# Optimization experiments

Hardware: AMD Instinct MI355X
Metric: run time of the kernel (lower is better)

Reference implementation:

```python
import jax, jax.numpy as jnp
import numpy as np

C = 27
SIZE = 448
PATCH = 14
G = PATCH * 4          # target_global = 56
SHN = (SIZE * SIZE) // (PATCH * PATCH)  # split_head_num = 1024
PW, GW = 0.75, 0.25    # patch_weight, global_weight
EPS = 1e-5


def setup_inputs() -> dict:
    key = jax.random.key(0)
    ks = jax.random.split(key, 9)
    s = 0.02
    return {
        "x": jax.random.normal(ks[0], (4, C, SIZE, SIZE), dtype=jnp.float32),
        "gn_w": jnp.ones((C,), jnp.float32),
        "gn_b": jnp.zeros((C,), jnp.float32),
        "q_w": jax.random.normal(ks[1], (C, C), jnp.float32) * s,
        "q_b": jax.random.normal(ks[2], (C,), jnp.float32) * s,
        "k_w": jax.random.normal(ks[3], (C, C), jnp.float32) * s,
        "k_b": jax.random.normal(ks[4], (C,), jnp.float32) * s,
        "v_w": jax.random.normal(ks[5], (C, C), jnp.float32) * s,
        "v_b": jax.random.normal(ks[6], (C,), jnp.float32) * s,
        "proj_w": jax.random.normal(ks[7], (C, C), jnp.float32) * s,
    }


def _conv1x1(w, bias, t):
    out = jnp.einsum('oc,bchw->bohw', w, t)
    return out if bias is None else out + bias[None, :, None, None]


def _bmm_attn(q, k, v, scale):
    # q,k,v: (b, d, n). w = softmax(q^T k * scale, axis=2); h = einsum over keys.
    w = jax.nn.softmax(jnp.einsum('bdn,bdm->bnm', q, k) * scale, axis=2)
    return jnp.einsum('bdj,bij->bdi', v, w)


def reference(x, gn_w, gn_b, q_w, q_b, k_w, k_b, v_w, v_b, proj_w):
    b, c, H, W = x.shape
    # GroupNorm(num_groups=1): normalize over (C,H,W) per sample
    mu = jnp.mean(x, axis=(1, 2, 3), keepdims=True)
    var = jnp.var(x, axis=(1, 2, 3), keepdims=True)
    xn = (x - mu) * jax.lax.rsqrt(var + EPS)
    xn = xn * gn_w[None, :, None, None] + gn_b[None, :, None, None]

    q = _conv1x1(q_w, q_b, xn)
    k = _conv1x1(k_w, k_b, xn)
    v = _conv1x1(v_w, v_b, xn)

    # AdaptiveAvgPool2d 448 -> 56 (exact factor 8): block mean
    f = H // G
    pool = lambda t: t.reshape(b, c, G, f, G, f).mean(axis=(3, 5))

    # patch-wise bmm attention: view (b, c*SHN, PATCH^2), attend over 196 positions
    d = c * SHN
    n = PATCH * PATCH
    qf = q.reshape(b, d, n)
    kf = k.reshape(b, d, n)
    vf = v.reshape(b, d, n)
    h_patch = _bmm_attn(qf, kf, vf, 1.0 / np.sqrt(d).astype(np.float32)).reshape(b, c, H, W)

    # global pooled bmm attention over 56*56 positions with dim c, then nearest upsample
    qg = pool(q).reshape(b, c, G * G)
    kg = pool(k).reshape(b, c, G * G)
    vg = pool(v).reshape(b, c, G * G)
    hg = _bmm_attn(qg, kg, vg, 1.0 / np.sqrt(c).astype(np.float32)).reshape(b, c, G, G)
    hg = jnp.repeat(jnp.repeat(hg, f, axis=2), f, axis=3)  # nearest upsample to (H, W)

    h_in = PW * h_patch + GW * hg
    return x + _conv1x1(proj_w, None, h_in)
```

## Files before the change

### kernel.cpp

```cpp
#include <hip/hip_runtime.h>
#include <hip/hip_bf16.h>
#include <cstdint>

namespace {
constexpr int BB = 4;
constexpr int CC = 27;
constexpr int HW = 448 * 448;
constexpr long long CHW = (long long)CC * HW;
constexpr int NP = 196;
constexpr int GG = 56 * 56;
constexpr int DTOT = CC * 1024;
constexpr float SCALE_P = 0.0060140449f;
constexpr float SCALE_G = 0.1924500897f;
constexpr float EPSV = 1e-5f;
constexpr int KCH = 512;
constexpr int NKS = DTOT / KCH;
constexpr int MPAD = 224;
constexpr int ROWB = 128;
constexpr int WFRAG = 7 * 13 * 64 * 8;
constexpr int XST = 40;
constexpr int GKC = 224;
constexpr int KST = 40;
constexpr int VST = 232;
constexpr int HST = 204;
}

typedef __attribute__((ext_vector_type(8))) short short8;
typedef __attribute__((ext_vector_type(4))) float f32x4;

__device__ __forceinline__ float bf2f(unsigned short u) {
    return __uint_as_float(((uint32_t)u) << 16);
}

__device__ __forceinline__ ushort f2bf(float f) {
    union { __hip_bfloat16 h; ushort u; } cv;
    cv.h = __float2bfloat16(f);
    return cv.u;
}

__global__ void k_fold(const float* __restrict__ pjw, const float* __restrict__ vw,
                       const float* __restrict__ vb, float* __restrict__ pvw,
                       float* __restrict__ pvb) {
    __shared__ float pj[729], vv[729], vbs[27];
    int t = threadIdx.x;
    for (int i = t; i < 729; i += 256) { pj[i] = pjw[i]; vv[i] = vw[i]; }
    if (t < 27) vbs[t] = vb[t];
    __syncthreads();
    for (int i = t; i < 729; i += 256) {
        int o = i / 27, c2 = i - (i / 27) * 27;
        float s = 0.f;
#pragma unroll
        for (int c = 0; c < 27; c++) s += pj[o * 27 + c] * vv[c * 27 + c2];
        pvw[i] = s;
    }
    if (t < 27) {
        float s = 0.f;
#pragma unroll
        for (int c = 0; c < 27; c++) s += pj[t * 27 + c] * vbs[c];
        pvb[t] = s;
    }
}

__global__ void k_gn_partial(const float* __restrict__ x, float* __restrict__ part) {
    int blk = blockIdx.x;
    int b = blk >> 10;
    int chunk = blk & 1023;
    const int CLEN = (int)(CHW / 1024);
    const float* p = x + (size_t)b * CHW + (size_t)chunk * CLEN;
    float s = 0.f, ss = 0.f;
    for (int i = threadIdx.x; i < CLEN; i += 256) {
        float v = p[i];
        s += v; ss += v * v;
    }
    for (int o = 32; o; o >>= 1) { s += __shfl_down(s, o); ss += __shfl_down(ss, o); }
    __shared__ float ls[4], lss[4];
    int wid = threadIdx.x >> 6, lane = threadIdx.x & 63;
    if (lane == 0) { ls[wid] = s; lss[wid] = ss; }
    __syncthreads();
    if (threadIdx.x == 0) {
        float S = ls[0] + ls[1] + ls[2] + ls[3];
        float SS = lss[0] + lss[1] + lss[2] + lss[3];
        part[blk * 2] = S; part[blk * 2 + 1] = SS;
    }
}

__global__ void k_gn_final(const float* __restrict__ part, float* __restrict__ stats) {
    int b = blockIdx.x;
    float s = 0.f, ss = 0.f;
    for (int i = threadIdx.x; i < 1024; i += 256) {
        s += part[(b * 1024 + i) * 2];
        ss += part[(b * 1024 + i) * 2 + 1];
    }
    for (int o = 32; o; o >>= 1) { s += __shfl_down(s, o); ss += __shfl_down(ss, o); }
    __shared__ float ls[4], lss[4];
    int wid = threadIdx.x >> 6, lane = threadIdx.x & 63;
    if (lane == 0) { ls[wid] = s; lss[wid] = ss; }
    __syncthreads();
    if (threadIdx.x == 0) {
        float S = ls[0] + ls[1] + ls[2] + ls[3];
        float SS = lss[0] + lss[1] + lss[2] + lss[3];
        float mean = S / (float)CHW;
        float var = SS / (float)CHW - mean * mean;
        stats[b * 2] = mean;
        stats[b * 2 + 1] = rsqrtf(var + EPSV);
    }
}

__global__ __launch_bounds__(256, 2)
void k_qkv_mfma(const float* __restrict__ x, const float* __restrict__ stats,
                const float* __restrict__ qw, const float* __restrict__ qb,
                const float* __restrict__ kw, const float* __restrict__ kb,
                const float* __restrict__ vw, const float* __restrict__ vb,
                const float* __restrict__ gnw, const float* __restrict__ gnb,
                __hip_bfloat16* __restrict__ qkv) {
    __shared__ ushort xs[256 * XST];
    __shared__ ushort wls[96 * XST];
    __shared__ __align__(16) float bls[96];
    __shared__ float gwls[27], gbls[27];

    int tid = threadIdx.x;
    int P0 = blockIdx.x * 256;
    int b = P0 / HW;
    int hw0 = P0 - b * HW;

    for (int i = tid; i < 96 * 32; i += 256) {
        int row = i >> 5, c = i & 31;
        float wv = 0.f;
        if (c < 27 && row < 81) {
            int t = (row >= 54) ? 2 : (row >= 27 ? 1 : 0);
            int oc = row - t * 27;
            const float* wp = (t == 0) ? qw : (t == 1) ? kw : vw;
            wv = wp[oc * 27 + c];
        }
        wls[row * XST + c] = f2bf(wv);
    }
    if (tid < 96) {
        float bv = 0.f;
        if (tid < 27) bv = qb[tid];
        else if (tid < 54) bv = kb[tid - 27];
        else if (tid < 81) bv = vb[tid - 54];
        bls[tid] = bv;
    }
    if (tid < 27) { gwls[tid] = gnw[tid]; gbls[tid] = gnb[tid]; }
    float mean = stats[b * 2], rstd = stats[b * 2 + 1];
    __syncthreads();

    {
        const float* xp = x + (size_t)b * CHW + hw0 + tid;
        ushort xv[28];
#pragma unroll
        for (int c = 0; c < 27; c++) {
            float v = (xp[(size_t)c * HW] - mean) * rstd * gwls[c] + gbls[c];
            xv[c] = f2bf(v);
        }
        xv[27] = 0;
        uint32_t* xrow = reinterpret_cast<uint32_t*>(&xs[tid * XST]);
#pragma unroll
        for (int i = 0; i < 14; i++)
            xrow[i] = (uint32_t)xv[2 * i] | ((uint32_t)xv[2 * i + 1] << 16);
        xrow[14] = 0; xrow[15] = 0;
    }
    __syncthreads();

    int w = tid >> 6, l = tid & 63;
    int lrow = l & 15, kg = l >> 4;

    short8 afr[6];
    f32x4 binit[6];
#pragma unroll
    for (int mt = 0; mt < 6; mt++) {
        afr[mt] = *reinterpret_cast<const short8*>(&wls[(mt * 16 + lrow) * XST + kg * 8]);
        binit[mt] = *reinterpret_cast<const f32x4*>(&bls[mt * 16 + kg * 4]);
    }

    f32x4 acc[4][6];
#pragma unroll
    for (int pt = 0; pt < 4; pt++) {
        const short8 bfr = *reinterpret_cast<const short8*>(
            &xs[(w * 64 + pt * 16 + lrow) * XST + kg * 8]);
#pragma unroll
        for (int mt = 0; mt < 6; mt++)
            acc[pt][mt] = __builtin_amdgcn_mfma_f32_16x16x32_bf16(afr[mt], bfr, binit[mt], 0, 0, 0);
    }

    ushort* ob = (ushort*)qkv;
#pragma unroll
    for (int pt = 0; pt < 4; pt++) {
        int hw = hw0 + w * 64 + pt * 16 + lrow;
#pragma unroll
        for (int mt = 0; mt < 6; mt++) {
#pragma unroll
            for (int r = 0; r < 4; r++) {
                int o = mt * 16 + kg * 4 + r;
                if (o < 81) {
                    int t = (o >= 54) ? 2 : (o >= 27 ? 1 : 0);
                    int oc = o - t * 27;
                    ob[((size_t)t * BB + b) * CHW + (size_t)oc * HW + hw] = f2bf(acc[pt][mt][r]);
                }
            }
        }
    }
}

__global__ void k_pool(const __hip_bfloat16* __restrict__ src, float* __restrict__ dst) {
    int idx = blockIdx.x * 256 + threadIdx.x;
    int g = idx % GG;
    int t = idx / GG;
    int c = t % 27;
    int b = t / 27;
    int gh = g / 56, gw = g - (g / 56) * 56;
    const ushort* sp = (const ushort*)src + (size_t)(b * 27 + c) * HW + (size_t)(gh * 8) * 448 + gw * 8;
    float s = 0.f;
#pragma unroll
    for (int r = 0; r < 8; r++) {
        const ushort4 a = *reinterpret_cast<const ushort4*>(sp + r * 448);
        const ushort4 d = *reinterpret_cast<const ushort4*>(sp + r * 448 + 4);
        s += bf2f(a.x) + bf2f(a.y) + bf2f(a.z) + bf2f(a.w)
           + bf2f(d.x) + bf2f(d.y) + bf2f(d.z) + bf2f(d.w);
    }
    dst[((size_t)b * GG + g) * 27 + c] = s * (1.f / 64.f);
}

__global__ __launch_bounds__(448, 1)
void k_spart_mfma(const __hip_bfloat16* __restrict__ q, const __hip_bfloat16* __restrict__ k,
                  float* __restrict__ spart) {
    __shared__ ushort lq[MPAD * 64];
    __shared__ ushort lk[MPAD * 64];
    int blk = blockIdx.x;
    int ks = blk % NKS;
    int b = blk / NKS;
    const ushort* qb_ = (const ushort*)q + (size_t)b * CHW;
    const ushort* kb_ = (const ushort*)k + (size_t)b * CHW;
    int t = threadIdx.x;
    int w = t >> 6, l = t & 63;
    int lrow = l & 15, lg = l >> 4;
    int sr = t & 15;
    int sn8 = t >> 4;

    f32x4 acc[2][13];
#pragma unroll
    for (int i = 0; i < 2; i++)
#pragma unroll
        for (int ct = 0; ct < 13; ct++) acc[i][ct] = (f32x4){0.f, 0.f, 0.f, 0.f};

    int d0 = ks * KCH;
    for (int step = 0; step < KCH / 32; ++step) {
        int dbase = d0 + step * 32;
        {
            const ushort* s0 = qb_ + (size_t)(dbase + 2 * sr) * NP + sn8 * 8;
            const ushort* s1 = s0 + NP;
            ushort4 a0 = *reinterpret_cast<const ushort4*>(s0);
            ushort4 a1 = *reinterpret_cast<const ushort4*>(s0 + 4);
            ushort4 b0 = *reinterpret_cast<const ushort4*>(s1);
            ushort4 b1 = *reinterpret_cast<const ushort4*>(s1 + 4);
            ushort ra[8] = {a0.x, a0.y, a0.z, a0.w, a1.x, a1.y, a1.z, a1.w};
            ushort rb[8] = {b0.x, b0.y, b0.z, b0.w, b1.x, b1.y, b1.z, b1.w};
#pragma unroll
            for (int kk = 0; kk < 8; kk++) {
                int n = sn8 * 8 + kk;
                uint32_t val = (uint32_t)ra[kk] | ((uint32_t)rb[kk] << 16);
                *reinterpret_cast<uint32_t*>(reinterpret_cast<char*>(lq) + n * ROWB +
                                             ((4 * sr) ^ (16 * (n & 7)))) = val;
            }
        }
        {
            const ushort* s0 = kb_ + (size_t)(dbase + 2 * sr) * NP + sn8 * 8;
            const ushort* s1 = s0 + NP;
            ushort4 a0 = *reinterpret_cast<const ushort4*>(s0);
            ushort4 a1 = *reinterpret_cast<const ushort4*>(s0 + 4);
            ushort4 b0 = *reinterpret_cast<const ushort4*>(s1);
            ushort4 b1 = *reinterpret_cast<const ushort4*>(s1 + 4);
            ushort ra[8] = {a0.x, a0.y, a0.z, a0.w, a1.x, a1.y, a1.z, a1.w};
            ushort rb[8] = {b0.x, b0.y, b0.z, b0.w, b1.x, b1.y, b1.z, b1.w};
#pragma unroll
            for (int kk = 0; kk < 8; kk++) {
                int m = sn8 * 8 + kk;
                uint32_t val = (uint32_t)ra[kk] | ((uint32_t)rb[kk] << 16);
                *reinterpret_cast<uint32_t*>(reinterpret_cast<char*>(lk) + m * ROWB +
                                             ((4 * sr) ^ (16 * (m & 7)))) = val;
            }
        }
        __syncthreads();
        int nA0 = (2 * w) * 16 + lrow;
        int nA1 = nA0 + 16;
        const short8 afr0 = *reinterpret_cast<const short8*>(
            reinterpret_cast<const char*>(lq) + nA0 * ROWB + 16 * (lg ^ (nA0 & 7)));
        const short8 afr1 = *reinterpret_cast<const short8*>(
            reinterpret_cast<const char*>(lq) + nA1 * ROWB + 16 * (lg ^ (nA1 & 7)));
#pragma unroll
        for (int ct = 0; ct < 13; ct++) {
            int m = ct * 16 + lrow;
            const short8 bfr = *reinterpret_cast<const short8*>(
                reinterpret_cast<const char*>(lk) + m * ROWB + 16 * (lg ^ (m & 7)));
            acc[0][ct] = __builtin_amdgcn_mfma_f32_16x16x32_bf16(afr0, bfr, acc[0][ct], 0, 0, 0);
            acc[1][ct] = __builtin_amdgcn_mfma_f32_16x16x32_bf16(afr1, bfr, acc[1][ct], 0, 0, 0);
        }
        __syncthreads();
    }
    float* sp = spart + (size_t)(b * NKS + ks) * NP * MPAD;
#pragma unroll
    for (int i = 0; i < 2; i++) {
        int rt = 2 * w + i;
#pragma unroll
        for (int r = 0; r < 4; r++) {
            int n = rt * 16 + lg * 4 + r;
            if (n < NP) {
#pragma unroll
                for (int ct = 0; ct < 13; ct++)
                    sp[(size_t)n * MPAD + ct * 16 + lrow] = acc[i][ct][r];
            }
        }
    }
}

__global__ void k_softmax(const float* __restrict__ spart, __hip_bfloat16* __restrict__ whf) {
    int blk = blockIdx.x;
    int n = blk % NP;
    int b = blk / NP;
    int m = threadIdx.x;
    float val = -1e30f;
    if (m < 196) {
        float s = 0.f;
        for (int ks = 0; ks < NKS; ks++)
            s += spart[((size_t)(b * NKS + ks) * NP + n) * MPAD + m];
        val = s * SCALE_P;
    }
    float mx = val;
    for (int o = 32; o; o >>= 1) mx = fmaxf(mx, __shfl_xor(mx, o));
    __shared__ float redm[4], reds[4];
    int wid = threadIdx.x >> 6, lane = threadIdx.x & 63;
    if (lane == 0) redm[wid] = mx;
    __syncthreads();
    mx = fmaxf(fmaxf(redm[0], redm[1]), fmaxf(redm[2], redm[3]));
    float p = (m < 196) ? __expf(val - mx) : 0.f;
    float sm = p;
    for (int o = 32; o; o >>= 1) sm += __shfl_xor(sm, o);
    if (lane == 0) reds[wid] = sm;
    __syncthreads();
    sm = reds[0] + reds[1] + reds[2] + reds[3];
    if (m < 224) {
        int ct = n >> 4, lr = n & 15;
        int step = m >> 5, kg = (m >> 3) & 3, e = m & 7;
        size_t addr = (size_t)b * WFRAG +
                      (((size_t)(step * 13 + ct) * 64 + kg * 16 + lr) << 3) + e;
        whf[addr] = __float2bfloat16((m < 196) ? p / sm : 0.f);
    }
}

__global__ __launch_bounds__(256)
void k_gattn_flash(const float* __restrict__ qg, const float* __restrict__ kg,
                   const float* __restrict__ vg, float* __restrict__ hg) {
    __shared__ __align__(16) ushort ksh[GKC * KST];
    __shared__ __align__(16) ushort vsh[32 * VST];
    __shared__ __align__(16) ushort psh[4][16 * VST];

    int blk = blockIdx.x;
    int b = blk / 49;
    int q0 = (blk % 49) * 64;
    int tid = threadIdx.x;
    int w = tid >> 6, l = tid & 63;
    int lr = l & 15, lg = l >> 4;

    for (int i = tid; i < GKC; i += 256) {
        ushort* kr = &ksh[i * KST];
        kr[27] = 0; kr[28] = 0; kr[29] = 0; kr[30] = 0; kr[31] = 0;
        vsh[27 * VST + i] = 0x3f80;
        vsh[28 * VST + i] = 0; vsh[29 * VST + i] = 0;
        vsh[30 * VST + i] = 0; vsh[31 * VST + i] = 0;
    }

    short8 aq;
    {
        const float* qr = qg + ((size_t)b * GG + q0 + w * 16 + lr) * 27;
#pragma unroll
        for (int j = 0; j < 8; j++) {
            int c = 8 * lg + j;
            aq[j] = (c < 27) ? (short)f2bf(qr[c]) : (short)0;
        }
    }

    f32x4 acc_h0 = {0.f, 0.f, 0.f, 0.f};
    f32x4 acc_h1 = {0.f, 0.f, 0.f, 0.f};
    ushort* myps = &psh[w][0];
    const float* kgb = kg + (size_t)b * GG * 27;
    const float* vgb = vg + (size_t)b * GG * 27;

    for (int ch = 0; ch < 14; ch++) {
        __syncthreads();
        int base = ch * GKC * 27;
        for (int idx = tid; idx < GKC * 27; idx += 256) {
            int kk = idx / 27, c = idx - (idx / 27) * 27;
            ksh[kk * KST + c] = f2bf(kgb[base + idx]);
            vsh[c * VST + kk] = f2bf(vgb[base + idx]);
        }
        __syncthreads();

        f32x4 s[14];
#pragma unroll
        for (int ct = 0; ct < 14; ct++) {
            const short8 bk = *reinterpret_cast<const short8*>(
                &ksh[(ct * 16 + lr) * KST + 8 * lg]);
            s[ct] = __builtin_amdgcn_mfma_f32_16x16x32_bf16(
                aq, bk, (f32x4){0.f, 0.f, 0.f, 0.f}, 0, 0, 0);
        }
#pragma unroll
        for (int ct = 0; ct < 14; ct++) {
#pragma unroll
            for (int r = 0; r < 4; r++) {
                float p = __expf(s[ct][r] * SCALE_G);
                myps[(4 * lg + r) * VST + ct * 16 + lr] = f2bf(p);
            }
        }
#pragma unroll
        for (int kstep = 0; kstep < 7; kstep++) {
            const short8 ap = *reinterpret_cast<const short8*>(
                &myps[lr * VST + kstep * 32 + 8 * lg]);
            const short8 bv0 = *reinterpret_cast<const short8*>(
                &vsh[lr * VST + kstep * 32 + 8 * lg]);
            const short8 bv1 = *reinterpret_cast<const short8*>(
                &vsh[(16 + lr) * VST + kstep * 32 + 8 * lg]);
            acc_h0 = __builtin_amdgcn_mfma_f32_16x16x32_bf16(ap, bv0, acc_h0, 0, 0, 0);
            acc_h1 = __builtin_amdgcn_mfma_f32_16x16x32_bf16(ap, bv1, acc_h1, 0, 0, 0);
        }
    }

#pragma unroll
    for (int r = 0; r < 4; r++) {
        float lsum = __shfl(acc_h1[r], (l & 48) | 11, 64);
        float inv = 1.f / lsum;
        int q = q0 + w * 16 + 4 * lg + r;
        float* hr = hg + ((size_t)b * GG + q) * 27;
        hr[lr] = acc_h0[r] * inv;
        if (lr < 11) hr[16 + lr] = acc_h1[r] * inv;
    }
}

__global__ __launch_bounds__(256)
void k_hp_fused(const __hip_bfloat16* __restrict__ v, const __hip_bfloat16* __restrict__ whf,
                const float* __restrict__ x, const float* __restrict__ hg,
                float* __restrict__ out) {
    __shared__ __align__(16) ushort hbuf[64 * HST];
    int blk = blockIdx.x;
    int b = blk / 432;
    int grp = blk % 432;
    int tid = threadIdx.x;
    int w = tid >> 6, l = tid & 63;
    int ar = l & 15;
    int kg = l >> 4;
    int D0 = (grp * 4 + w) * 16;

    const ushort* vb = (const ushort*)v + (size_t)b * CHW;
    const ushort* wf = (const ushort*)whf + (size_t)b * WFRAG;

    const ushort* arow = vb + (size_t)(D0 + ar) * NP;
    short8 av[7];
#pragma unroll
    for (int step = 0; step < 7; ++step) {
        int joff = step * 32 + kg * 8;
        ushort4 alo = *reinterpret_cast<const ushort4*>(arow + joff);
        ushort4 ahi = *reinterpret_cast<const ushort4*>(arow + joff + 4);
        av[step][0] = alo.x; av[step][1] = alo.y; av[step][2] = alo.z; av[step][3] = alo.w;
        av[step][4] = ahi.x; av[step][5] = ahi.y; av[step][6] = ahi.z; av[step][7] = ahi.w;
    }

    f32x4 acc[13];
#pragma unroll
    for (int ct = 0; ct < 13; ct++) acc[ct] = (f32x4){0.f, 0.f, 0.f, 0.f};

#pragma unroll
    for (int step = 0; step < 7; ++step) {
        short8 bv[13];
#pragma unroll
        for (int ct = 0; ct < 13; ct++)
            bv[ct] = *reinterpret_cast<const short8*>(
                wf + (((size_t)(step * 13 + ct) * 64 + l) << 3));
#pragma unroll
        for (int ct = 0; ct < 13; ct++)
            acc[ct] = __builtin_amdgcn_mfma_f32_16x16x32_bf16(av[step], bv[ct], acc[ct], 0, 0, 0);
    }

#pragma unroll
    for (int ct = 0; ct < 13; ct++) {
        int i = ct * 16 + ar;
        if (i < NP) {
#pragma unroll
            for (int r = 0; r < 4; r++)
                hbuf[(w * 16 + kg * 4 + r) * HST + i] = f2bf(acc[ct][r]);
        }
    }
    __syncthreads();

    int c = grp >> 4;
    int pix0 = (grp & 15) * 64 * NP;
    const float* xb = x + (size_t)b * CHW + (size_t)c * HW + pix0;
    float* ob = out + (size_t)b * CHW + (size_t)c * HW + pix0;
    const float* hgb = hg + (size_t)b * GG * 27;
    for (int idx4 = tid; idx4 < 3136; idx4 += 256) {
        int j = idx4 * 4;
        int sl = j / NP;
        int i = j - sl * NP;
        ushort4 hv = *reinterpret_cast<const ushort4*>(&hbuf[sl * HST + i]);
        int pix = pix0 + j;
        int h = pix / 448;
        int w2 = pix - h * 448;
        int g = (h >> 3) * 56 + (w2 >> 3);
        float hgs = 0.25f * hgb[g * 27 + c];
        float4 xv = *reinterpret_cast<const float4*>(&xb[j]);
        float4 ov;
        ov.x = xv.x + 0.75f * bf2f(hv.x) + hgs;
        ov.y = xv.y + 0.75f * bf2f(hv.y) + hgs;
        ov.z = xv.z + 0.75f * bf2f(hv.z) + hgs;
        ov.w = xv.w + 0.75f * bf2f(hv.w) + hgs;
        *reinterpret_cast<float4*>(&ob[j]) = ov;
    }
}

extern "C" void kernel_launch(void* const* d_in, const int* in_sizes, int n_in,
                              void* d_out, int out_size, void* d_ws, size_t ws_size,
                              hipStream_t stream) {
    const float* x    = (const float*)d_in[0];
    const float* gnw  = (const float*)d_in[1];
    const float* gnb  = (const float*)d_in[2];
    const float* qw   = (const float*)d_in[3];
    const float* qb   = (const float*)d_in[4];
    const float* kw   = (const float*)d_in[5];
    const float* kb   = (const float*)d_in[6];
    const float* vw   = (const float*)d_in[7];
    const float* vb   = (const float*)d_in[8];
    const float* pjw  = (const float*)d_in[9];
    float* out = (float*)d_out;

    char* ws = (char*)d_ws;
    size_t off = 0;
    auto alloc = [&](size_t bytes) { void* p = ws + off; off += (bytes + 255) & ~(size_t)255; return p; };
    __hip_bfloat16* qkvbuf = (__hip_bfloat16*)alloc((size_t)3 * BB * CHW * 2 + 64);
    __hip_bfloat16* qbf = qkvbuf;
    __hip_bfloat16* kbf = qkvbuf + (size_t)BB * CHW;
    __hip_bfloat16* vbf = qkvbuf + (size_t)2 * BB * CHW;
    float* spart = (float*)alloc((size_t)BB * NKS * NP * MPAD * 4);
    __hip_bfloat16* wHat = (__hip_bfloat16*)alloc((size_t)BB * WFRAG * 2);
    float* qg    = (float*)alloc((size_t)BB * GG * 27 * 4);
    float* kg    = (float*)alloc((size_t)BB * GG * 27 * 4);
    float* vg    = (float*)alloc((size_t)BB * GG * 27 * 4);
    float* hg    = (float*)alloc((size_t)BB * GG * 27 * 4);
    float* part  = (float*)alloc((size_t)BB * 1024 * 2 * 4);
    float* stats = (float*)alloc((size_t)BB * 2 * 4);
    float* pvw   = (float*)alloc(729 * 4);
    float* pvb   = (float*)alloc(27 * 4);

    (void)hipMemsetAsync((char*)qkvbuf + (size_t)3 * BB * CHW * 2, 0, 64, stream);
    k_fold<<<1, 256, 0, stream>>>(pjw, vw, vb, pvw, pvb);
    k_gn_partial<<<BB * 1024, 256, 0, stream>>>(x, part);
    k_gn_final<<<BB, 256, 0, stream>>>(part, stats);
    k_qkv_mfma<<<(BB * HW) / 256, 256, 0, stream>>>(x, stats, qw, qb, kw, kb, pvw, pvb,
                                                    gnw, gnb, qkvbuf);
    k_pool<<<(BB * 27 * GG) / 256, 256, 0, stream>>>(qbf, qg);
    k_pool<<<(BB * 27 * GG) / 256, 256, 0, stream>>>(kbf, kg);
    k_pool<<<(BB * 27 * GG) / 256, 256, 0, stream>>>(vbf, vg);
    k_spart_mfma<<<BB * NKS, 448, 0, stream>>>(qbf, kbf, spart);
    k_softmax<<<BB * NP, 256, 0, stream>>>(spart, wHat);
    k_gattn_flash<<<BB * 49, 256, 0, stream>>>(qg, kg, vg, hg);
    k_hp_fused<<<BB * 432, 256, 0, stream>>>(vbf, wHat, x, hg, out);
}
```

Measured before the change: 294.6 us.

## Prefetch residual x before MFMA and remap block order across XCDs

The fused output kernel now loads its 12 float4 slices of the residual x into registers at kernel start, so that global load latency overlaps with the V·W MFMA work instead of sitting after the barrier. The block index is also permuted so that consecutive hardware block IDs, which are dealt round-robin to the 8 XCDs, map to contiguous work chunks per XCD, aiming for better L2 locality. The cost is 48 extra live VGPRs across the MFMA section, which may lower occupancy. The remap assumes the grid size is divisible by 8.

```diff
diff --git a/kernel.cpp b/kernel.cpp
--- a/kernel.cpp
+++ b/kernel.cpp
@@ -440,7 +440,9 @@
                 const float* __restrict__ x, const float* __restrict__ hg,
                 float* __restrict__ out) {
     __shared__ __align__(16) ushort hbuf[64 * HST];
-    int blk = blockIdx.x;
+    int nper = gridDim.x >> 3;
+    int bid = blockIdx.x;
+    int blk = (bid & 7) * nper + (bid >> 3);
     int b = blk / 432;
     int grp = blk % 432;
     int tid = threadIdx.x;
@@ -449,6 +451,14 @@
     int kg = l >> 4;
     int D0 = (grp * 4 + w) * 16;
 
+    int c = grp >> 4;
+    int pix0 = (grp & 15) * 64 * NP;
+    const float* xb = x + (size_t)b * CHW + (size_t)c * HW + pix0;
+    float4 xpre[12];
+#pragma unroll
+    for (int it = 0; it < 12; ++it)
+        xpre[it] = *reinterpret_cast<const float4*>(&xb[(tid + it * 256) * 4]);
+
     const ushort* vb = (const ushort*)v + (size_t)b * CHW;
     const ushort* wf = (const ushort*)whf + (size_t)b * WFRAG;
 
@@ -490,12 +500,30 @@
     }
     __syncthreads();
 
-    int c = grp >> 4;
-    int pix0 = (grp & 15) * 64 * NP;
-    const float* xb = x + (size_t)b * CHW + (size_t)c * HW + pix0;
     float* ob = out + (size_t)b * CHW + (size_t)c * HW + pix0;
     const float* hgb = hg + (size_t)b * GG * 27;
-    for (int idx4 = tid; idx4 < 3136; idx4 += 256) {
+#pragma unroll
+    for (int it = 0; it < 12; ++it) {
+        int idx4 = tid + it * 256;
+        int j = idx4 * 4;
+        int sl = j / NP;
+        int i = j - sl * NP;
+        ushort4 hv = *reinterpret_cast<const ushort4*>(&hbuf[sl * HST + i]);
+        int pix = pix0 + j;
+        int h = pix / 448;
+        int w2 = pix - h * 448;
+        int g = (h >> 3) * 56 + (w2 >> 3);
+        float hgs = 0.25f * hgb[g * 27 + c];
+        float4 xv = xpre[it];
+        float4 ov;
+        ov.x = xv.x + 0.75f * bf2f(hv.x) + hgs;
+        ov.y = xv.y + 0.75f * bf2f(hv.y) + hgs;
+        ov.z = xv.z + 0.75f * bf2f(hv.z) + hgs;
+        ov.w = xv.w + 0.75f * bf2f(hv.w) + hgs;
+        *reinterpret_cast<float4*>(&ob[j]) = ov;
+    }
+    if (tid < 64) {
+        int idx4 = 3072 + tid;
         int j = idx4 * 4;
         int sl = j / NP;
         int i = j - sl * NP;
```

Measured after the change: 282.1 us. 1.04x faster.
